# Optimization experiments

Measured on AMD Instinct MI355X. Metric: run time of the kernel, lower is better.

The kernel has to match this reference:

```python
import jax, jax.numpy as jnp
import numpy as np

N = 100000
E = 1600000
EPS = 1e-5


def gcn_conv(x, W, b, rows, cols, w):
    # x: [N, Fin], rows/cols: [E+N] (self-loops included), w: [E+N]
    h = x @ W  # [N, Fout]
    deg = jax.ops.segment_sum(w, cols, num_segments=N)  # [N]
    dinv = jnp.where(deg > 0, jax.lax.rsqrt(deg), 0.0)
    coef = dinv[rows] * w * dinv[cols]  # [E+N]
    out = jax.ops.segment_sum(coef[:, None] * h[rows], cols, num_segments=N)
    return out + b


def batch_norm(x, g, be):
    mu = jnp.mean(x, axis=0)
    var = jnp.mean(jnp.square(x - mu), axis=0)  # biased, as torch BN
    return (x - mu) * jax.lax.rsqrt(var + EPS) * g + be


def setup_inputs() -> dict:
    key = jax.random.key(0)
    ks = jax.random.split(key, 8)
    x = jax.random.normal(ks[0], (N, 256), dtype=jnp.float32)
    edge_index = jax.random.randint(ks[1], (2, E), 0, N, dtype=jnp.int64)
    edge_weight = jax.random.uniform(ks[2], (E,), dtype=jnp.float32)
    W1 = jax.random.normal(ks[3], (256, 128), dtype=jnp.float32) * (1.0 / np.sqrt(256))
    W2 = jax.random.normal(ks[4], (128, 128), dtype=jnp.float32) * (1.0 / np.sqrt(128))
    W3 = jax.random.normal(ks[5], (128, 64), dtype=jnp.float32) * (1.0 / np.sqrt(128))
    return {
        "x": x, "edge_index": edge_index, "edge_weight": edge_weight,
        "W1": W1, "b1": jnp.zeros(128), "g1": jnp.ones(128), "be1": jnp.zeros(128),
        "W2": W2, "b2": jnp.zeros(128), "g2": jnp.ones(128), "be2": jnp.zeros(128),
        "W3": W3, "b3": jnp.zeros(64),
    }


def reference(x, edge_index, edge_weight, W1, b1, g1, be1, W2, b2, g2, be2, W3, b3):
    # add self-loops (weight 1.0), as PyG GCNConv default
    loops = jnp.arange(N, dtype=edge_index.dtype)
    rows = jnp.concatenate([edge_index[0], loops])
    cols = jnp.concatenate([edge_index[1], loops])
    w = jnp.concatenate([edge_weight, jnp.ones((N,), dtype=edge_weight.dtype)])

    h = gcn_conv(x, W1, b1, rows, cols, w)
    h = jax.nn.relu(batch_norm(h, g1, be1))  # dropout is identity (eval)
    h = gcn_conv(h, W2, b2, rows, cols, w)
    h = jax.nn.relu(batch_norm(h, g2, be2))
    out = gcn_conv(h, W3, b3, rows, cols, w)
    return out
```

## Files before the change

kernel.cpp:

```cpp
#include <hip/hip_runtime.h>
#include <cstddef>


#define WS_ALIGN(x) (((x) + 255) & ~(size_t)255)

__global__ __launch_bounds__(256) void init_kernel(unsigned long long* packed,
                                                   float* sums, float* sumsq,
                                                   int N) {
  int i = blockIdx.x * 256 + threadIdx.x;
  if (i < N) packed[i] = 0ull;
  if (i < 128) { sums[i] = 0.f; sumsq[i] = 0.f; }
}

__global__ __launch_bounds__(256) void edge_deg_kernel(const int* __restrict__ cols,
                                                       const float* __restrict__ w,
                                                       unsigned long long* __restrict__ packed,
                                                       int E) {
  int e = blockIdx.x * 256 + threadIdx.x;
  if (e >= E) return;
  int c = cols[e];
  unsigned long long v = (1ull << 40) |
                         (unsigned long long)(unsigned int)__float2uint_rn(w[e] * 1048576.0f);
  atomicAdd(&packed[c], v);
}

__global__ __launch_bounds__(256) void dinv_kernel(const unsigned long long* __restrict__ packed,
                                                   float* __restrict__ dinv, int N) {
  int i = blockIdx.x * 256 + threadIdx.x;
  if (i < N) {
    float deg = 1.0f + (float)(packed[i] & 0xFFFFFFFFFFull) * (1.0f / 1048576.0f);
    dinv[i] = rsqrtf(deg);
  }
}

__global__ __launch_bounds__(256) void scan1_kernel(const unsigned long long* __restrict__ packed,
                                                    int* __restrict__ bsum, int N) {
  int base = blockIdx.x * 2048 + threadIdx.x * 8;
  int s = 0;
#pragma unroll
  for (int j = 0; j < 8; ++j) { int i = base + j; if (i < N) s += (int)(packed[i] >> 40); }
  __shared__ int ls[256];
  ls[threadIdx.x] = s; __syncthreads();
  for (int st = 128; st > 0; st >>= 1) {
    if (threadIdx.x < st) ls[threadIdx.x] += ls[threadIdx.x + st];
    __syncthreads();
  }
  if (threadIdx.x == 0) bsum[blockIdx.x] = ls[0];
}

__global__ void scan2_kernel(const int* __restrict__ bsum, int* __restrict__ bpref,
                             int nb, int* __restrict__ offsets, int N) {
  int lane = threadIdx.x;
  int mine = (lane < nb) ? bsum[lane] : 0;
  int v = mine;
  for (int st = 1; st < 64; st <<= 1) {
    int t = __shfl_up(v, st, 64);
    if (lane >= st) v += t;
  }
  if (lane < nb) bpref[lane] = v - mine;
  if (lane == 63) offsets[N] = v;
}

__global__ __launch_bounds__(256) void scan3_kernel(const unsigned long long* __restrict__ packed,
                                                    const int* __restrict__ bpref,
                                                    int* __restrict__ offsets,
                                                    int* __restrict__ cursors, int N) {
  int tid = threadIdx.x;
  int base = blockIdx.x * 2048 + tid * 8;
  int v[8]; int s = 0;
#pragma unroll
  for (int j = 0; j < 8; ++j) {
    int i = base + j;
    v[j] = (i < N) ? (int)(packed[i] >> 40) : 0;
    s += v[j];
  }
  __shared__ int ls[256];
  ls[tid] = s; __syncthreads();
  for (int st = 1; st < 256; st <<= 1) {
    int t = (tid >= st) ? ls[tid - st] : 0;
    __syncthreads();
    ls[tid] += t;
    __syncthreads();
  }
  int run = bpref[blockIdx.x] + (ls[tid] - s);
#pragma unroll
  for (int j = 0; j < 8; ++j) {
    int i = base + j;
    if (i < N) { offsets[i] = run; cursors[i] = run; run += v[j]; }
  }
}

__global__ __launch_bounds__(256) void scatter_kernel(const int* __restrict__ rows,
                                                      const int* __restrict__ cols,
                                                      const float* __restrict__ w,
                                                      const float* __restrict__ dinv,
                                                      int* __restrict__ cursors,
                                                      int* __restrict__ srow,
                                                      float* __restrict__ scoef, int E) {
  int e = blockIdx.x * 256 + threadIdx.x;
  if (e >= E) return;
  int r = rows[e], c = cols[e];
  int pos = atomicAdd(&cursors[c], 1);
  srow[pos] = r;
  scoef[pos] = dinv[r] * w[e] * dinv[c];
}

template <int K, int F, int BM, int TM, bool PRO>
__global__ __launch_bounds__(256)
void gemm_kernel(const float* __restrict__ A, const float* __restrict__ W,
                 float* __restrict__ out, int M,
                 const float* __restrict__ alpha, const float* __restrict__ beta) {
  constexpr int BK = 32;
  constexpr int TN = 8;
  constexpr int TX = F / TN;
  constexpr int TY = BM / TM;
  static_assert(TX * TY == 256, "bad tile config");
  static_assert(TM == 4 || TM == 8, "TM must be 4 or 8");
  __shared__ float As[BK][BM + 1];
  __shared__ float Bs[BK][F];
  const int tid = threadIdx.x;
  const int tx = tid % TX;
  const int ty = tid / TX;
  const int row0 = blockIdx.x * BM;
  float acc[TM][TN];
#pragma unroll
  for (int m = 0; m < TM; ++m)
#pragma unroll
    for (int n = 0; n < TN; ++n) acc[m][n] = 0.f;

  const int ar = tid >> 3;
  const int ak = (tid & 7) * 4;

  for (int k0 = 0; k0 < K; k0 += BK) {
#pragma unroll
    for (int p = 0; p < BM / 32; ++p) {
      int r = p * 32 + ar;
      int gr = row0 + r;
      float4 v;
      if (gr < M) v = *(const float4*)(A + (size_t)gr * K + k0 + ak);
      else        v = make_float4(0.f, 0.f, 0.f, 0.f);
      if constexpr (PRO) {
        float4 al = *(const float4*)(alpha + k0 + ak);
        float4 be = *(const float4*)(beta + k0 + ak);
        v.x = fmaxf(fmaf(v.x, al.x, be.x), 0.f);
        v.y = fmaxf(fmaf(v.y, al.y, be.y), 0.f);
        v.z = fmaxf(fmaf(v.z, al.z, be.z), 0.f);
        v.w = fmaxf(fmaf(v.w, al.w, be.w), 0.f);
      }
      As[ak + 0][r] = v.x; As[ak + 1][r] = v.y;
      As[ak + 2][r] = v.z; As[ak + 3][r] = v.w;
    }
#pragma unroll
    for (int p = 0; p < (BK * F) / 1024; ++p) {
      int idx = p * 256 + tid;
      int kk = idx / (F / 4);
      int cc = (idx % (F / 4)) * 4;
      *(float4*)&Bs[kk][cc] = *(const float4*)(W + (size_t)(k0 + kk) * F + cc);
    }
    __syncthreads();
#pragma unroll
    for (int kk = 0; kk < BK; ++kk) {
      float a[TM], b[TN];
      *(float4*)&a[0] = *(const float4*)&As[kk][ty * 4];
      if constexpr (TM == 8)
        *(float4*)&a[4] = *(const float4*)&As[kk][BM / 2 + ty * 4];
      *(float4*)&b[0] = *(const float4*)&Bs[kk][tx * 4];
      *(float4*)&b[4] = *(const float4*)&Bs[kk][F / 2 + tx * 4];
#pragma unroll
      for (int m = 0; m < TM; ++m)
#pragma unroll
        for (int n = 0; n < TN; ++n)
          acc[m][n] = fmaf(a[m], b[n], acc[m][n]);
    }
    __syncthreads();
  }
#pragma unroll
  for (int m = 0; m < TM; ++m) {
    int gr = row0 + ((TM == 8 && m >= 4) ? (BM / 2 + ty * 4 + m - 4) : (ty * 4 + m));
    if (gr < M) {
      float4* o0 = (float4*)(out + (size_t)gr * F + tx * 4);
      float4* o1 = (float4*)(out + (size_t)gr * F + F / 2 + tx * 4);
      *o0 = make_float4(acc[m][0], acc[m][1], acc[m][2], acc[m][3]);
      *o1 = make_float4(acc[m][4], acc[m][5], acc[m][6], acc[m][7]);
    }
  }
}

template <int F>
__global__ __launch_bounds__(256)
void agg_kernel(const float* __restrict__ h, const int* __restrict__ srow,
                const float* __restrict__ scoef, const int* __restrict__ off,
                const float* __restrict__ dinv, const float* __restrict__ bias,
                float* __restrict__ out, int N) {
  constexpr int VPL = F / 64;
  int wid = blockIdx.x * 4 + (threadIdx.x >> 6);
  if (wid >= N) return;
  int lane = threadIdx.x & 63;
  float d = dinv[wid];
  float acc[VPL];
  {
    const float* hc = h + (size_t)wid * F;
#pragma unroll
    for (int j = 0; j < VPL; ++j)
      acc[j] = d * d * hc[lane * VPL + j] + bias[lane * VPL + j];
  }
  int s = off[wid], e = off[wid + 1];
  int i = s;
  for (; i + 4 <= e; i += 4) {
    int r0 = srow[i], r1 = srow[i + 1], r2 = srow[i + 2], r3 = srow[i + 3];
    float c0 = scoef[i], c1 = scoef[i + 1], c2 = scoef[i + 2], c3 = scoef[i + 3];
    const float* h0 = h + (size_t)r0 * F;
    const float* h1 = h + (size_t)r1 * F;
    const float* h2 = h + (size_t)r2 * F;
    const float* h3 = h + (size_t)r3 * F;
    float v0[VPL], v1[VPL], v2[VPL], v3[VPL];
#pragma unroll
    for (int j = 0; j < VPL; ++j) v0[j] = h0[lane * VPL + j];
#pragma unroll
    for (int j = 0; j < VPL; ++j) v1[j] = h1[lane * VPL + j];
#pragma unroll
    for (int j = 0; j < VPL; ++j) v2[j] = h2[lane * VPL + j];
#pragma unroll
    for (int j = 0; j < VPL; ++j) v3[j] = h3[lane * VPL + j];
#pragma unroll
    for (int j = 0; j < VPL; ++j) acc[j] = fmaf(c0, v0[j], acc[j]);
#pragma unroll
    for (int j = 0; j < VPL; ++j) acc[j] = fmaf(c1, v1[j], acc[j]);
#pragma unroll
    for (int j = 0; j < VPL; ++j) acc[j] = fmaf(c2, v2[j], acc[j]);
#pragma unroll
    for (int j = 0; j < VPL; ++j) acc[j] = fmaf(c3, v3[j], acc[j]);
  }
  for (; i < e; ++i) {
    int r0 = srow[i]; float c0 = scoef[i];
    const float* h0 = h + (size_t)r0 * F;
#pragma unroll
    for (int j = 0; j < VPL; ++j) acc[j] = fmaf(c0, h0[lane * VPL + j], acc[j]);
  }
  float* oc = out + (size_t)wid * F;
#pragma unroll
  for (int j = 0; j < VPL; ++j) oc[lane * VPL + j] = acc[j];
}

__global__ __launch_bounds__(256) void stats_kernel(const float* __restrict__ x, int N,
                                                    float* __restrict__ sums,
                                                    float* __restrict__ sumsq) {
  int f = threadIdx.x & 127;
  int half = threadIdx.x >> 7;
  int rend = min(N, (int)(blockIdx.x + 1) * 64);
  float s = 0.f, ss = 0.f;
  for (int r = blockIdx.x * 64 + half; r < rend; r += 2) {
    float v = x[(size_t)r * 128 + f];
    s += v; ss += v * v;
  }
  __shared__ float ls[256], lss[256];
  ls[threadIdx.x] = s; lss[threadIdx.x] = ss;
  __syncthreads();
  if (half == 0) {
    s += ls[threadIdx.x + 128];
    ss += lss[threadIdx.x + 128];
    atomicAdd(&sums[f], s);
    atomicAdd(&sumsq[f], ss);
  }
}

__global__ void finalize_kernel(const float* __restrict__ g, const float* __restrict__ be,
                                float* __restrict__ sums, float* __restrict__ sumsq,
                                float* __restrict__ alpha, float* __restrict__ beta,
                                float invN) {
  int f = threadIdx.x;
  float mu = sums[f] * invN;
  float var = sumsq[f] * invN - mu * mu;
  float a = g[f] * rsqrtf(var + 1e-5f);
  alpha[f] = a;
  beta[f] = be[f] - mu * a;
  sums[f] = 0.f; sumsq[f] = 0.f;
}

extern "C" void kernel_launch(void* const* d_in, const int* in_sizes, int n_in,
                              void* d_out, int out_size, void* d_ws, size_t ws_size,
                              hipStream_t stream) {
  const float* x   = (const float*)d_in[0];
  const int*   ei  = (const int*)d_in[1];
  const float* ew  = (const float*)d_in[2];
  const float* W1  = (const float*)d_in[3];
  const float* b1  = (const float*)d_in[4];
  const float* g1  = (const float*)d_in[5];
  const float* be1 = (const float*)d_in[6];
  const float* W2  = (const float*)d_in[7];
  const float* b2  = (const float*)d_in[8];
  const float* g2  = (const float*)d_in[9];
  const float* be2 = (const float*)d_in[10];
  const float* W3  = (const float*)d_in[11];
  const float* b3  = (const float*)d_in[12];

  const int N = in_sizes[0] / 256;
  const int E = in_sizes[2];
  const int* rows = ei;
  const int* cols = ei + E;

  char* p = (char*)d_ws;
  auto carve = [&](size_t bytes) { char* q = p; p += WS_ALIGN(bytes); return (void*)q; };
  unsigned long long* packed = (unsigned long long*)carve((size_t)N * 8);
  float* dinv    = (float*)carve((size_t)N * 4);
  int*   offsets = (int*)  carve(((size_t)N + 1) * 4);
  int*   cursors = (int*)  carve((size_t)N * 4);
  int*   bsum    = (int*)  carve(256 * 4);
  int*   bpref   = (int*)  carve(256 * 4);
  int*   srow    = (int*)  carve((size_t)E * 4);
  float* scoef   = (float*)carve((size_t)E * 4);
  float* h       = (float*)carve((size_t)N * 128 * 4);
  float* agg     = (float*)carve((size_t)N * 128 * 4);
  float* sums    = (float*)carve(128 * 4);
  float* sumsq   = (float*)carve(128 * 4);
  float* alpha   = (float*)carve(128 * 4);
  float* beta    = (float*)carve(128 * 4);
  (void)ws_size; (void)n_in; (void)out_size;

  const int gN = (N + 255) / 256;
  const int gE = (E + 255) / 256;
  const int nb = (N + 2047) / 2048;

  init_kernel<<<gN, 256, 0, stream>>>(packed, sums, sumsq, N);
  edge_deg_kernel<<<gE, 256, 0, stream>>>(cols, ew, packed, E);
  dinv_kernel<<<gN, 256, 0, stream>>>(packed, dinv, N);
  scan1_kernel<<<nb, 256, 0, stream>>>(packed, bsum, N);
  scan2_kernel<<<1, 64, 0, stream>>>(bsum, bpref, nb, offsets, N);
  scan3_kernel<<<nb, 256, 0, stream>>>(packed, bpref, offsets, cursors, N);
  scatter_kernel<<<gE, 256, 0, stream>>>(rows, cols, ew, dinv, cursors, srow, scoef, E);

  const int gAgg = (N + 3) / 4;
  const int gG = (N + 127) / 128;

  gemm_kernel<256, 128, 128, 8, false><<<gG, 256, 0, stream>>>(x, W1, h, N, nullptr, nullptr);
  agg_kernel<128><<<gAgg, 256, 0, stream>>>(h, srow, scoef, offsets, dinv, b1, agg, N);
  stats_kernel<<<(N + 63) / 64, 256, 0, stream>>>(agg, N, sums, sumsq);
  finalize_kernel<<<1, 128, 0, stream>>>(g1, be1, sums, sumsq, alpha, beta, 1.0f / (float)N);

  gemm_kernel<128, 128, 128, 8, true><<<gG, 256, 0, stream>>>(agg, W2, h, N, alpha, beta);
  agg_kernel<128><<<gAgg, 256, 0, stream>>>(h, srow, scoef, offsets, dinv, b2, agg, N);
  stats_kernel<<<(N + 63) / 64, 256, 0, stream>>>(agg, N, sums, sumsq);
  finalize_kernel<<<1, 128, 0, stream>>>(g2, be2, sums, sumsq, alpha, beta, 1.0f / (float)N);

  gemm_kernel<128, 64, 128, 4, true><<<gG, 256, 0, stream>>>(agg, W3, h, N, alpha, beta);
  agg_kernel<64><<<gAgg, 256, 0, stream>>>(h, srow, scoef, offsets, dinv, b3, (float*)d_out, N);
}
```

Measured before the change: 1.079 ms.

## Prefetch next GEMM tile into registers and shrink tiles for occupancy

The GEMM kernel now loads the next K-tile from global memory into registers while computing on the current shared-memory tile, then writes it to shared memory after a barrier. This hides global load latency behind FMA work. The per-thread tile also shrinks to 4 rows, with BM of 64 for the 128-wide layers and launch bounds requesting 4 blocks per CU, to raise occupancy. The cost is more register pressure from the prefetch buffers, less reuse per thread, and more blocks.

```diff
diff --git a/kernel.cpp b/kernel.cpp
--- a/kernel.cpp
+++ b/kernel.cpp
@@ -105,17 +105,18 @@
   scoef[pos] = dinv[r] * w[e] * dinv[c];
 }
 
-template <int K, int F, int BM, int TM, bool PRO>
-__global__ __launch_bounds__(256)
+template <int K, int F, int BM, bool PRO>
+__global__ __launch_bounds__(256, 4)
 void gemm_kernel(const float* __restrict__ A, const float* __restrict__ W,
                  float* __restrict__ out, int M,
                  const float* __restrict__ alpha, const float* __restrict__ beta) {
   constexpr int BK = 32;
-  constexpr int TN = 8;
+  constexpr int TM = 4, TN = 8;
   constexpr int TX = F / TN;
   constexpr int TY = BM / TM;
+  constexpr int NA = BM / 32;
+  constexpr int NB = (BK * F) / 1024;
   static_assert(TX * TY == 256, "bad tile config");
-  static_assert(TM == 4 || TM == 8, "TM must be 4 or 8");
   __shared__ float As[BK][BM + 1];
   __shared__ float Bs[BK][F];
   const int tid = threadIdx.x;
@@ -131,39 +132,56 @@
   const int ar = tid >> 3;
   const int ak = (tid & 7) * 4;
 
-  for (int k0 = 0; k0 < K; k0 += BK) {
-#pragma unroll
-    for (int p = 0; p < BM / 32; ++p) {
-      int r = p * 32 + ar;
-      int gr = row0 + r;
-      float4 v;
-      if (gr < M) v = *(const float4*)(A + (size_t)gr * K + k0 + ak);
-      else        v = make_float4(0.f, 0.f, 0.f, 0.f);
-      if constexpr (PRO) {
-        float4 al = *(const float4*)(alpha + k0 + ak);
-        float4 be = *(const float4*)(beta + k0 + ak);
-        v.x = fmaxf(fmaf(v.x, al.x, be.x), 0.f);
-        v.y = fmaxf(fmaf(v.y, al.y, be.y), 0.f);
-        v.z = fmaxf(fmaf(v.z, al.z, be.z), 0.f);
-        v.w = fmaxf(fmaf(v.w, al.w, be.w), 0.f);
-      }
-      As[ak + 0][r] = v.x; As[ak + 1][r] = v.y;
-      As[ak + 2][r] = v.z; As[ak + 3][r] = v.w;
-    }
-#pragma unroll
-    for (int p = 0; p < (BK * F) / 1024; ++p) {
+  float4 rA[NA], rB[NB], rAl, rBe;
+
+  auto load_tile = [&](int k0) {
+#pragma unroll
+    for (int p = 0; p < NA; ++p) {
+      int gr = row0 + p * 32 + ar;
+      rA[p] = (gr < M) ? *(const float4*)(A + (size_t)gr * K + k0 + ak)
+                       : make_float4(0.f, 0.f, 0.f, 0.f);
+    }
+#pragma unroll
+    for (int p = 0; p < NB; ++p) {
       int idx = p * 256 + tid;
       int kk = idx / (F / 4);
       int cc = (idx % (F / 4)) * 4;
-      *(float4*)&Bs[kk][cc] = *(const float4*)(W + (size_t)(k0 + kk) * F + cc);
-    }
-    __syncthreads();
+      rB[p] = *(const float4*)(W + (size_t)(k0 + kk) * F + cc);
+    }
+    if constexpr (PRO) {
+      rAl = *(const float4*)(alpha + k0 + ak);
+      rBe = *(const float4*)(beta + k0 + ak);
+    }
+  };
+
+  auto store_tile = [&]() {
+#pragma unroll
+    for (int p = 0; p < NA; ++p) {
+      float4 v = rA[p];
+      if constexpr (PRO) {
+        v.x = fmaxf(fmaf(v.x, rAl.x, rBe.x), 0.f);
+        v.y = fmaxf(fmaf(v.y, rAl.y, rBe.y), 0.f);
+        v.z = fmaxf(fmaf(v.z, rAl.z, rBe.z), 0.f);
+        v.w = fmaxf(fmaf(v.w, rAl.w, rBe.w), 0.f);
+      }
+      int r = p * 32 + ar;
+      As[ak + 0][r] = v.x; As[ak + 1][r] = v.y;
+      As[ak + 2][r] = v.z; As[ak + 3][r] = v.w;
+    }
+#pragma unroll
+    for (int p = 0; p < NB; ++p) {
+      int idx = p * 256 + tid;
+      int kk = idx / (F / 4);
+      int cc = (idx % (F / 4)) * 4;
+      *(float4*)&Bs[kk][cc] = rB[p];
+    }
+  };
+
+  auto compute = [&]() {
 #pragma unroll
     for (int kk = 0; kk < BK; ++kk) {
       float a[TM], b[TN];
       *(float4*)&a[0] = *(const float4*)&As[kk][ty * 4];
-      if constexpr (TM == 8)
-        *(float4*)&a[4] = *(const float4*)&As[kk][BM / 2 + ty * 4];
       *(float4*)&b[0] = *(const float4*)&Bs[kk][tx * 4];
       *(float4*)&b[4] = *(const float4*)&Bs[kk][F / 2 + tx * 4];
 #pragma unroll
@@ -172,11 +190,23 @@
         for (int n = 0; n < TN; ++n)
           acc[m][n] = fmaf(a[m], b[n], acc[m][n]);
     }
-    __syncthreads();
-  }
+  };
+
+  load_tile(0);
+  store_tile();
+  __syncthreads();
+  for (int k0 = BK; k0 < K; k0 += BK) {
+    load_tile(k0);
+    compute();
+    __syncthreads();
+    store_tile();
+    __syncthreads();
+  }
+  compute();
+
 #pragma unroll
   for (int m = 0; m < TM; ++m) {
-    int gr = row0 + ((TM == 8 && m >= 4) ? (BM / 2 + ty * 4 + m - 4) : (ty * 4 + m));
+    int gr = row0 + ty * 4 + m;
     if (gr < M) {
       float4* o0 = (float4*)(out + (size_t)gr * F + tx * 4);
       float4* o1 = (float4*)(out + (size_t)gr * F + F / 2 + tx * 4);
@@ -330,18 +360,17 @@
   scatter_kernel<<<gE, 256, 0, stream>>>(rows, cols, ew, dinv, cursors, srow, scoef, E);
 
   const int gAgg = (N + 3) / 4;
-  const int gG = (N + 127) / 128;
-
-  gemm_kernel<256, 128, 128, 8, false><<<gG, 256, 0, stream>>>(x, W1, h, N, nullptr, nullptr);
+
+  gemm_kernel<256, 128, 64, false><<<(N + 63) / 64, 256, 0, stream>>>(x, W1, h, N, nullptr, nullptr);
   agg_kernel<128><<<gAgg, 256, 0, stream>>>(h, srow, scoef, offsets, dinv, b1, agg, N);
   stats_kernel<<<(N + 63) / 64, 256, 0, stream>>>(agg, N, sums, sumsq);
   finalize_kernel<<<1, 128, 0, stream>>>(g1, be1, sums, sumsq, alpha, beta, 1.0f / (float)N);
 
-  gemm_kernel<128, 128, 128, 8, true><<<gG, 256, 0, stream>>>(agg, W2, h, N, alpha, beta);
+  gemm_kernel<128, 128, 64, true><<<(N + 63) / 64, 256, 0, stream>>>(agg, W2, h, N, alpha, beta);
   agg_kernel<128><<<gAgg, 256, 0, stream>>>(h, srow, scoef, offsets, dinv, b2, agg, N);
   stats_kernel<<<(N + 63) / 64, 256, 0, stream>>>(agg, N, sums, sumsq);
   finalize_kernel<<<1, 128, 0, stream>>>(g2, be2, sums, sumsq, alpha, beta, 1.0f / (float)N);
 
-  gemm_kernel<128, 64, 128, 4, true><<<gG, 256, 0, stream>>>(agg, W3, h, N, alpha, beta);
+  gemm_kernel<128, 64, 128, true><<<(N + 127) / 128, 256, 0, stream>>>(agg, W3, h, N, alpha, beta);
   agg_kernel<64><<<gAgg, 256, 0, stream>>>(h, srow, scoef, offsets, dinv, b3, (float*)d_out, N);
 }
```

New measurement: 2.232 ms. 2.07x slower.
